# Optimization experiments

Measured on AMD Instinct MI355X. Metric: run time of the kernel, lower is better.

The kernel has to match this reference:

```python
import jax, jax.numpy as jnp
import numpy as np

LN_EPS = 1e-5

def _layernorm(x, g, b):
    mu = jnp.mean(x, axis=-1, keepdims=True)
    var = jnp.mean(jnp.square(x - mu), axis=-1, keepdims=True)
    return (x - mu) * jax.lax.rsqrt(var + LN_EPS) * g + b


def setup_inputs() -> dict:
    key = jax.random.key(0)
    ks = jax.random.split(key, 8)
    B, N, F = 2, 100000, 128
    E, G = 400000, 10
    EMB, C = 32, 128
    features = jax.random.normal(ks[0], (B, N, F), dtype=jnp.float32)
    edge_index = jax.random.randint(ks[1], (2, E), 0, N, dtype=jnp.int32)
    lengths = jnp.full((G,), N // G, dtype=jnp.int32)
    emb_table = jax.random.normal(ks[2], (128, EMB), dtype=jnp.float32)
    W_in = jax.random.normal(ks[3], (F - 1 + EMB, C), dtype=jnp.float32) * (1.0 / np.sqrt(F - 1 + EMB))
    b_in = jnp.zeros((C,), jnp.float32)
    g_in = jnp.ones((C,), jnp.float32)
    beta_in = jnp.zeros((C,), jnp.float32)
    msg_W = jax.random.normal(ks[4], (3, C, C), dtype=jnp.float32) * (1.0 / np.sqrt(C))
    msg_b = jnp.zeros((3, C), jnp.float32)
    msg_g = jnp.ones((3, C), jnp.float32)
    msg_beta = jnp.zeros((3, C), jnp.float32)
    W_proj = jax.random.normal(ks[5], (C, 1), dtype=jnp.float32) * (1.0 / np.sqrt(C))
    b_proj = jnp.zeros((1,), jnp.float32)
    return {"features": features, "edge_index": edge_index, "lengths": lengths,
            "emb_table": emb_table, "W_in": W_in, "b_in": b_in, "g_in": g_in, "beta_in": beta_in,
            "msg_W": msg_W, "msg_b": msg_b, "msg_g": msg_g, "msg_beta": msg_beta,
            "W_proj": W_proj, "b_proj": b_proj}


def reference(features, edge_index, lengths, emb_table, W_in, b_in, g_in, beta_in,
              msg_W, msg_b, msg_g, msg_beta, W_proj, b_proj):
    B, N, F = features.shape
    rows, cols = edge_index[0], edge_index[1]

    # row-normalized sparse adjacency values (no grad path in original: torch.no_grad)
    ones = jnp.ones(rows.shape[0], dtype=features.dtype)
    deg = jax.ops.segment_sum(ones, rows, num_segments=N)
    vals = 1.0 / jnp.clip(deg, 1.0)[rows]  # [E]
    vals = jax.lax.stop_gradient(vals)

    # embedding input layer
    op = jnp.clip(features[..., 0].astype(jnp.int32), 0, emb_table.shape[0] - 1)  # [B,N]
    x = jnp.concatenate([emb_table[op], features[..., 1:]], axis=-1)  # [B,N,F-1+emb]
    x = _layernorm(jax.nn.silu(x @ W_in + b_in), g_in, beta_in)  # [B,N,C]

    # sparse message passing: agg[i] = sum_j A[i,j] x[j]
    for l in range(msg_W.shape[0]):
        msg = x[:, cols, :] * vals[None, :, None]  # [B,E,C]
        agg = jnp.zeros_like(x).at[:, rows, :].add(msg)  # scatter-sum to rows
        x = _layernorm(jax.nn.silu(agg @ msg_W[l] + msg_b[l]), msg_g[l], msg_beta[l])

    # ragged graph pooling over node axis
    G = lengths.shape[0]
    index = jnp.asarray(np.repeat(np.arange(G), np.asarray(lengths)))  # [N]
    pooled = jax.ops.segment_sum(x.transpose(1, 0, 2), index, num_segments=G)  # [G,B,C]
    runtimes = pooled @ W_proj + b_proj  # [G,B,1]
    return runtimes[..., 0]  # [G,B]
```

## Files before the change

kernel.cpp:

```cpp
#include <hip/hip_runtime.h>
#include <cstddef>

#define LN_EPS 1e-5f
typedef unsigned short u16;
typedef unsigned int u32;
typedef __attribute__((ext_vector_type(8))) short bf16x8;
typedef __attribute__((ext_vector_type(4))) float f32x4;

constexpr int SCAN_T = 256, SCAN_V = 8, SCAN_ELEMS = SCAN_T * SCAN_V;
constexpr int KP = 136;

__device__ inline u16 f2bf(float f) {
    u32 u = __float_as_uint(f);
    u += 0x7FFFu + ((u >> 16) & 1u);
    return (u16)(u >> 16);
}
__device__ inline float bf2f(u16 h) { return __uint_as_float((u32)h << 16); }

__device__ inline void acc_u4(float* a, uint4 u) {
    a[0] += bf2f((u16)(u.x & 0xFFFF)); a[1] += bf2f((u16)(u.x >> 16));
    a[2] += bf2f((u16)(u.y & 0xFFFF)); a[3] += bf2f((u16)(u.y >> 16));
    a[4] += bf2f((u16)(u.z & 0xFFFF)); a[5] += bf2f((u16)(u.z >> 16));
    a[6] += bf2f((u16)(u.w & 0xFFFF)); a[7] += bf2f((u16)(u.w >> 16));
}

__global__ __launch_bounds__(256) void k_deg(const int* __restrict__ rows,
                                             int* __restrict__ deg, int E) {
    int e = blockIdx.x * 256 + threadIdx.x;
    if (e < E) atomicAdd(&deg[rows[e]], 1);
}

__global__ __launch_bounds__(256) void k_invdeg(const int* __restrict__ deg,
                                                float* __restrict__ invdeg, int N) {
    int i = blockIdx.x * 256 + threadIdx.x;
    if (i < N) invdeg[i] = 1.0f / (float)max(deg[i], 1);
}

__global__ __launch_bounds__(SCAN_T) void k_scan1(const int* __restrict__ deg,
                                                  int* __restrict__ row_ptr,
                                                  int* __restrict__ bsum, int N) {
    __shared__ int ts[SCAN_T];
    int t = threadIdx.x;
    int base = blockIdx.x * SCAN_ELEMS;
    int v[SCAN_V];
    int s = 0;
    #pragma unroll
    for (int j = 0; j < SCAN_V; ++j) {
        int i = base + t * SCAN_V + j;
        v[j] = (i < N) ? deg[i] : 0;
        s += v[j];
    }
    ts[t] = s;
    __syncthreads();
    for (int off = 1; off < SCAN_T; off <<= 1) {
        int val = (t >= off) ? ts[t - off] : 0;
        __syncthreads();
        ts[t] += val;
        __syncthreads();
    }
    int excl = (t > 0) ? ts[t - 1] : 0;
    #pragma unroll
    for (int j = 0; j < SCAN_V; ++j) {
        int i = base + t * SCAN_V + j;
        if (i < N) row_ptr[i] = excl;
        excl += v[j];
    }
    if (t == SCAN_T - 1) bsum[blockIdx.x] = ts[SCAN_T - 1];
}

__global__ void k_scan2(int* __restrict__ bsum, int nb, int* __restrict__ row_ptr, int N) {
    int run = 0;
    for (int i = 0; i < nb; ++i) {
        int v = bsum[i];
        bsum[i] = run;
        run += v;
    }
    row_ptr[N] = run;
}

__global__ __launch_bounds__(SCAN_T) void k_scan3(int* __restrict__ row_ptr,
                                                  const int* __restrict__ bsum, int N) {
    int add = bsum[blockIdx.x];
    int base = blockIdx.x * SCAN_ELEMS;
    #pragma unroll
    for (int j = 0; j < SCAN_V; ++j) {
        int i = base + threadIdx.x * SCAN_V + j;
        if (i < N) row_ptr[i] += add;
    }
}

__global__ __launch_bounds__(256) void k_copy_cursor(const int* __restrict__ row_ptr,
                                                     int* __restrict__ cursor, int N) {
    int i = blockIdx.x * 256 + threadIdx.x;
    if (i < N) cursor[i] = row_ptr[i];
}

__global__ __launch_bounds__(256) void k_bucket(const int* __restrict__ rows,
                                                const int* __restrict__ cols,
                                                int* __restrict__ cursor,
                                                int* __restrict__ col_sorted, int E) {
    int e = blockIdx.x * 256 + threadIdx.x;
    if (e < E) {
        int r = rows[e];
        int pos = atomicAdd(&cursor[r], 1);
        col_sorted[pos] = cols[e];
    }
}

__global__ __launch_bounds__(256) void k_wprep(const float* __restrict__ W_in,
                                               const float* __restrict__ msg_W,
                                               u16* __restrict__ Wt_in,
                                               u16* __restrict__ Wt_msg) {
    int idx = blockIdx.x * 256 + threadIdx.x;
    const int t1 = 128 * 128;
    if (idx < t1) {
        int c = idx >> 7, k = idx & 127;
        float v = (k >= 1) ? W_in[(31 + k) * 128 + c] : 0.f;
        Wt_in[idx] = f2bf(v);
    } else {
        idx -= t1;
        if (idx < 3 * 128 * 128) {
            int l = idx / (128 * 128);
            int r = idx & (128 * 128 - 1);
            int c = r >> 7, k = r & 127;
            Wt_msg[idx] = f2bf(msg_W[l * 16384 + k * 128 + c]);
        }
    }
}

__global__ __launch_bounds__(128) void k_eproj(const float* __restrict__ W_in,
                                               const float* __restrict__ emb,
                                               float* __restrict__ E_proj) {
    __shared__ float es[32];
    int op = blockIdx.x, c = threadIdx.x;
    if (c < 32) es[c] = emb[op * 32 + c];
    __syncthreads();
    float s = 0.f;
    #pragma unroll
    for (int j = 0; j < 32; ++j) s = fmaf(es[j], W_in[j * 128 + c], s);
    E_proj[op * 128 + c] = s;
}

__global__ __launch_bounds__(256) void k_input_mfma(
    const float* __restrict__ features, const float* __restrict__ E_proj,
    const u16* __restrict__ Wt,
    const float* __restrict__ bias, const float* __restrict__ gain,
    const float* __restrict__ beta, u16* __restrict__ x, int N, int ntiles)
{
    __shared__ u16 A[64 * KP];
    __shared__ u16 Wl[128 * KP];
    __shared__ int ops[64];
    const int tid = threadIdx.x;
    const int lane = tid & 63, w = tid >> 6;
    const int l15 = lane & 15;
    const int kq = (lane >> 4) * 8;
    const int r = tid >> 2, q = tid & 3;

    for (int i = tid; i < 2048; i += 256) {
        uint4 v = ((const uint4*)Wt)[i];
        *(uint4*)&Wl[(i >> 4) * KP + (i & 15) * 8] = v;
    }
    float bsr[8], gsr[8], btr[8];
    #pragma unroll
    for (int t = 0; t < 8; ++t) {
        int col = t * 16 + l15;
        bsr[t] = bias[col]; gsr[t] = gain[col]; btr[t] = beta[col];
    }

    for (int tile = blockIdx.x; tile < ntiles; tile += gridDim.x) {
        const int node0 = tile * 32;
        __syncthreads();
        {
            int nl = r >> 1, b = r & 1;
            int node = min(node0 + nl, N - 1);
            const float* fr = features + ((size_t)b * N + node) * 128 + q * 32;
            u32 pk[16];
            float4 v0 = ((const float4*)fr)[0];
            if (q == 0) {
                int op = (int)v0.x;
                op = op < 0 ? 0 : (op > 127 ? 127 : op);
                ops[r] = op;
            }
            pk[0] = (u32)f2bf(v0.x) | ((u32)f2bf(v0.y) << 16);
            pk[1] = (u32)f2bf(v0.z) | ((u32)f2bf(v0.w) << 16);
            #pragma unroll
            for (int j = 1; j < 8; ++j) {
                float4 v = ((const float4*)fr)[j];
                pk[2 * j]     = (u32)f2bf(v.x) | ((u32)f2bf(v.y) << 16);
                pk[2 * j + 1] = (u32)f2bf(v.z) | ((u32)f2bf(v.w) << 16);
            }
            uint4* dst = (uint4*)&A[r * KP + q * 32];
            #pragma unroll
            for (int j = 0; j < 4; ++j)
                dst[j] = make_uint4(pk[4 * j], pk[4 * j + 1], pk[4 * j + 2], pk[4 * j + 3]);
        }
        __syncthreads();

        const int arow = w * 16 + l15;
        bf16x8 a[4];
        #pragma unroll
        for (int kt = 0; kt < 4; ++kt)
            a[kt] = *(const bf16x8*)&A[arow * KP + kt * 32 + kq];
        f32x4 acc[8];
        #pragma unroll
        for (int t = 0; t < 8; ++t) {
            f32x4 c4 = {0.f, 0.f, 0.f, 0.f};
            #pragma unroll
            for (int kt = 0; kt < 4; ++kt) {
                bf16x8 b = *(const bf16x8*)&Wl[(t * 16 + l15) * KP + kt * 32 + kq];
                c4 = __builtin_amdgcn_mfma_f32_16x16x32_bf16(a[kt], b, c4, 0, 0, 0);
            }
            acc[t] = c4;
        }

        int opr[4];
        #pragma unroll
        for (int i = 0; i < 4; ++i) opr[i] = ops[w * 16 + (lane >> 4) * 4 + i];

        float s[4] = {0, 0, 0, 0}, sq[4] = {0, 0, 0, 0};
        #pragma unroll
        for (int t = 0; t < 8; ++t) {
            int col = t * 16 + l15;
            #pragma unroll
            for (int i = 0; i < 4; ++i) {
                float aY = acc[t][i] + bsr[t] + E_proj[opr[i] * 128 + col];
                float y = aY / (1.0f + __expf(-aY));
                acc[t][i] = y;
                s[i] += y;
                sq[i] = fmaf(y, y, sq[i]);
            }
        }
        #pragma unroll
        for (int m = 1; m <= 8; m <<= 1) {
            #pragma unroll
            for (int i = 0; i < 4; ++i) {
                s[i] += __shfl_xor(s[i], m);
                sq[i] += __shfl_xor(sq[i], m);
            }
        }
        #pragma unroll
        for (int i = 0; i < 4; ++i) {
            float mu = s[i] * (1.0f / 128.0f);
            float var = sq[i] * (1.0f / 128.0f) - mu * mu;
            float inv = rsqrtf(var + LN_EPS);
            int rr = w * 16 + (lane >> 4) * 4 + i;
            if (node0 + (rr >> 1) < N) {
                u16* xr = x + ((size_t)node0 * 2 + rr) * 128;
                #pragma unroll
                for (int t = 0; t < 8; ++t)
                    xr[t * 16 + l15] = f2bf((acc[t][i] - mu) * inv * gsr[t] + btr[t]);
            }
        }
    }
}

__global__ __launch_bounds__(512) void k_mp_mfma(
    const int* __restrict__ row_ptr, const int* __restrict__ col_sorted,
    const float* __restrict__ invdeg, const u16* __restrict__ xin,
    const u16* __restrict__ Wt, const float* __restrict__ bias,
    const float* __restrict__ gain, const float* __restrict__ beta,
    u16* __restrict__ xout, int N, int ntiles)
{
    __shared__ u16 A[64 * KP];
    __shared__ u16 Wl[128 * KP];
    __shared__ float pS[64][2], pQ[64][2];
    const int tid = threadIdx.x;
    const int lane = tid & 63, w = tid >> 6;
    const int l15 = lane & 15;
    const int kq = (lane >> 4) * 8;
    const int r = tid >> 3, sl = tid & 7;
    const int wr = w & 3, wc = w >> 2;

    for (int i = tid; i < 2048; i += 512) {
        uint4 v = ((const uint4*)Wt)[i];
        *(uint4*)&Wl[(i >> 4) * KP + (i & 15) * 8] = v;
    }

    for (int tile = blockIdx.x; tile < ntiles; tile += gridDim.x) {
        const int node0 = tile * 32;
        {
            int nl = r >> 1, b = r & 1;
            int node = min(node0 + nl, N - 1);
            int e0 = row_ptr[node], e1 = row_ptr[node + 1];
            float sc = invdeg[node];
            const u32* xb = (const u32*)xin + (size_t)b * 64 + sl * 8;
            float fa[16];
            #pragma unroll
            for (int j = 0; j < 16; ++j) fa[j] = 0.f;
            int e = e0;
            for (; e + 2 <= e1; e += 2) {
                int c0 = col_sorted[e], c1 = col_sorted[e + 1];
                const uint4* p0 = (const uint4*)(xb + (size_t)c0 * 128);
                const uint4* p1 = (const uint4*)(xb + (size_t)c1 * 128);
                uint4 u0 = p0[0], u1 = p0[1];
                uint4 w0 = p1[0], w1 = p1[1];
                acc_u4(fa, u0);     acc_u4(fa + 8, u1);
                acc_u4(fa, w0);     acc_u4(fa + 8, w1);
            }
            if (e < e1) {
                const uint4* p0 = (const uint4*)(xb + (size_t)col_sorted[e] * 128);
                uint4 u0 = p0[0], u1 = p0[1];
                acc_u4(fa, u0);     acc_u4(fa + 8, u1);
            }
            u32 pk[8];
            #pragma unroll
            for (int j = 0; j < 8; ++j)
                pk[j] = (u32)f2bf(fa[2 * j] * sc) | ((u32)f2bf(fa[2 * j + 1] * sc) << 16);
            uint4* dst = (uint4*)&A[r * KP + sl * 16];
            dst[0] = make_uint4(pk[0], pk[1], pk[2], pk[3]);
            dst[1] = make_uint4(pk[4], pk[5], pk[6], pk[7]);
        }
        __syncthreads();

        const int arow = wr * 16 + l15;
        bf16x8 a[4];
        #pragma unroll
        for (int kt = 0; kt < 4; ++kt)
            a[kt] = *(const bf16x8*)&A[arow * KP + kt * 32 + kq];
        f32x4 acc[4];
        #pragma unroll
        for (int t = 0; t < 4; ++t) {
            int bcol = wc * 64 + t * 16 + l15;
            f32x4 c4 = {0.f, 0.f, 0.f, 0.f};
            #pragma unroll
            for (int kt = 0; kt < 4; ++kt) {
                bf16x8 bfr = *(const bf16x8*)&Wl[bcol * KP + kt * 32 + kq];
                c4 = __builtin_amdgcn_mfma_f32_16x16x32_bf16(a[kt], bfr, c4, 0, 0, 0);
            }
            acc[t] = c4;
        }

        float s[4] = {0, 0, 0, 0}, sq[4] = {0, 0, 0, 0};
        #pragma unroll
        for (int t = 0; t < 4; ++t) {
            int col = wc * 64 + t * 16 + l15;
            float bt = bias[col];
            #pragma unroll
            for (int i = 0; i < 4; ++i) {
                float aY = acc[t][i] + bt;
                float y = aY / (1.0f + __expf(-aY));
                acc[t][i] = y;
                s[i] += y;
                sq[i] = fmaf(y, y, sq[i]);
            }
        }
        #pragma unroll
        for (int m = 1; m <= 8; m <<= 1) {
            #pragma unroll
            for (int i = 0; i < 4; ++i) {
                s[i] += __shfl_xor(s[i], m);
                sq[i] += __shfl_xor(sq[i], m);
            }
        }
        if (l15 == 0) {
            #pragma unroll
            for (int i = 0; i < 4; ++i) {
                int rr = wr * 16 + (lane >> 4) * 4 + i;
                pS[rr][wc] = s[i];
                pQ[rr][wc] = sq[i];
            }
        }
        __syncthreads();

        #pragma unroll
        for (int i = 0; i < 4; ++i) {
            int rr = wr * 16 + (lane >> 4) * 4 + i;
            float st = pS[rr][0] + pS[rr][1];
            float qt = pQ[rr][0] + pQ[rr][1];
            float mu = st * (1.0f / 128.0f);
            float var = qt * (1.0f / 128.0f) - mu * mu;
            float inv = rsqrtf(var + LN_EPS);
            if (node0 + (rr >> 1) < N) {
                u16* xr = xout + ((size_t)node0 * 2 + rr) * 128;
                #pragma unroll
                for (int t = 0; t < 4; ++t) {
                    int col = wc * 64 + t * 16 + l15;
                    xr[col] = f2bf((acc[t][i] - mu) * inv * gain[col] + beta[col]);
                }
            }
        }
    }
}

__global__ __launch_bounds__(64) void k_pool(
    const u16* __restrict__ x, const int* __restrict__ lengths,
    float* __restrict__ pooled, int N, int B, int G, int SPLIT)
{
    int blk = blockIdx.x;
    int split = blk % SPLIT;
    int gb = blk / SPLIT;
    int b = gb % B, g = gb / B;
    int lane = threadIdx.x;
    int start = 0;
    for (int i = 0; i < g; ++i) start += lengths[i];
    int len = lengths[g];
    int chunk = (len + SPLIT - 1) / SPLIT;
    int n0 = start + split * chunk;
    int n1 = min(start + len, n0 + chunk);
    const u32* xb = (const u32*)x + (size_t)b * 64;
    float sx = 0.f, sy = 0.f;
    int n = n0;
    for (; n + 4 <= n1; n += 4) {
        u32 v0 = xb[(size_t)(n + 0) * 128 + lane];
        u32 v1 = xb[(size_t)(n + 1) * 128 + lane];
        u32 v2 = xb[(size_t)(n + 2) * 128 + lane];
        u32 v3 = xb[(size_t)(n + 3) * 128 + lane];
        sx += bf2f((u16)(v0 & 0xFFFF)) + bf2f((u16)(v1 & 0xFFFF)) +
              bf2f((u16)(v2 & 0xFFFF)) + bf2f((u16)(v3 & 0xFFFF));
        sy += bf2f((u16)(v0 >> 16)) + bf2f((u16)(v1 >> 16)) +
              bf2f((u16)(v2 >> 16)) + bf2f((u16)(v3 >> 16));
    }
    for (; n < n1; ++n) {
        u32 v = xb[(size_t)n * 128 + lane];
        sx += bf2f((u16)(v & 0xFFFF));
        sy += bf2f((u16)(v >> 16));
    }
    if (n1 > n0) {
        atomicAdd(&pooled[(g * B + b) * 128 + lane * 2 + 0], sx);
        atomicAdd(&pooled[(g * B + b) * 128 + lane * 2 + 1], sy);
    }
}

__global__ __launch_bounds__(128) void k_proj(
    const float* __restrict__ pooled, const float* __restrict__ Wp,
    const float* __restrict__ bp, float* __restrict__ out, int GB)
{
    int gb = blockIdx.x;
    int tid = threadIdx.x;
    float v = pooled[gb * 128 + tid] * Wp[tid];
    v += __shfl_down(v, 32);
    v += __shfl_down(v, 16);
    v += __shfl_down(v, 8);
    v += __shfl_down(v, 4);
    v += __shfl_down(v, 2);
    v += __shfl_down(v, 1);
    __shared__ float red[2];
    if ((tid & 63) == 0) red[tid >> 6] = v;
    __syncthreads();
    if (tid == 0) out[gb] = red[0] + red[1] + bp[0];
}

extern "C" void kernel_launch(void* const* d_in, const int* in_sizes, int n_in,
                              void* d_out, int out_size, void* d_ws, size_t ws_size,
                              hipStream_t stream) {
    const float* features = (const float*)d_in[0];
    const int* edge_index = (const int*)d_in[1];
    const int* lengths    = (const int*)d_in[2];
    const float* emb      = (const float*)d_in[3];
    const float* W_in     = (const float*)d_in[4];
    const float* b_in     = (const float*)d_in[5];
    const float* g_in     = (const float*)d_in[6];
    const float* beta_in  = (const float*)d_in[7];
    const float* msg_W    = (const float*)d_in[8];
    const float* msg_b    = (const float*)d_in[9];
    const float* msg_g    = (const float*)d_in[10];
    const float* msg_beta = (const float*)d_in[11];
    const float* W_proj   = (const float*)d_in[12];
    const float* b_proj   = (const float*)d_in[13];
    float* out = (float*)d_out;

    const int E = in_sizes[1] / 2;
    const int G = in_sizes[2];
    const int B = out_size / G;
    const int C = in_sizes[5];
    const int F = 128;
    const int N = in_sizes[0] / (B * F);
    const int M = B * N;
    const int L = in_sizes[9] / C;

    const int* rows = edge_index;
    const int* cols = edge_index + E;

    u16* buf0   = (u16*)d_ws;
    u16* buf1   = buf0 + (size_t)M * 128;
    u16* Wt_in  = buf1 + (size_t)M * 128;
    u16* Wt_msg = Wt_in + 128 * 128;
    float* E_proj = (float*)(Wt_msg + 3 * 128 * 128);
    float* invdeg = E_proj + 128 * 128;
    int*   deg    = (int*)(invdeg + N);
    float* pooled = (float*)(deg + N);
    int*   row_ptr = (int*)(pooled + (size_t)G * B * 128);
    int*   col_sorted = row_ptr + N + 1;
    int*   bsum   = col_sorted + E;

    const int nb_scan = (N + SCAN_ELEMS - 1) / SCAN_ELEMS;
    const int nt32 = (N + 31) / 32;
    const int grid_mp = nt32 < 1024 ? nt32 : 1024;

    {
        int total = 4 * 128 * 128;
        k_wprep<<<(total + 255) / 256, 256, 0, stream>>>(W_in, msg_W, Wt_in, Wt_msg);
        k_eproj<<<128, 128, 0, stream>>>(W_in, emb, E_proj);
    }

    hipMemsetAsync(deg, 0, (size_t)N * sizeof(int), stream);
    k_deg<<<(E + 255) / 256, 256, 0, stream>>>(rows, deg, E);
    k_invdeg<<<(N + 255) / 256, 256, 0, stream>>>(deg, invdeg, N);
    k_scan1<<<nb_scan, SCAN_T, 0, stream>>>(deg, row_ptr, bsum, N);
    k_scan2<<<1, 1, 0, stream>>>(bsum, nb_scan, row_ptr, N);
    k_scan3<<<nb_scan, SCAN_T, 0, stream>>>(row_ptr, bsum, N);
    k_copy_cursor<<<(N + 255) / 256, 256, 0, stream>>>(row_ptr, deg, N);
    k_bucket<<<(E + 255) / 256, 256, 0, stream>>>(rows, cols, deg, col_sorted, E);

    k_input_mfma<<<grid_mp, 256, 0, stream>>>(features, E_proj, Wt_in,
                                              b_in, g_in, beta_in, buf0, N, nt32);

    u16* bufs[2] = {buf0, buf1};
    int cur = 0;
    for (int l = 0; l < L; ++l) {
        k_mp_mfma<<<grid_mp, 512, 0, stream>>>(row_ptr, col_sorted, invdeg,
                                               bufs[cur], Wt_msg + (size_t)l * 128 * 128,
                                               msg_b + (size_t)l * C, msg_g + (size_t)l * C,
                                               msg_beta + (size_t)l * C,
                                               bufs[1 - cur], N, nt32);
        cur = 1 - cur;
    }

    const int SPLIT = 128;
    hipMemsetAsync(pooled, 0, (size_t)G * B * 128 * sizeof(float), stream);
    k_pool<<<G * B * SPLIT, 64, 0, stream>>>(bufs[cur], lengths, pooled, N, B, G, SPLIT);
    k_proj<<<G * B, 128, 0, stream>>>(pooled, W_proj, b_proj, out, G * B);
}
```

Measured before the change: 338.0 us.

## Split input-layer columns across two wave groups with 512-thread blocks

The input MFMA kernel moves from 256 to 512 threads per block. Each wave now computes 64 of the 128 output columns for 16 rows, and the feature load is spread over 8 threads per row instead of 4. LayerNorm row statistics are combined across the two column halves through shared memory with an added barrier, and the barrier at the top of the tile loop is dropped. The aim is more parallelism and less register pressure per thread, at the cost of a shared-memory reduction and bias/gain/beta reads from global memory inside the loop instead of registers.

```diff
diff --git a/kernel.cpp b/kernel.cpp
--- a/kernel.cpp
+++ b/kernel.cpp
@@ -141,7 +141,7 @@
     E_proj[op * 128 + c] = s;
 }
 
-__global__ __launch_bounds__(256) void k_input_mfma(
+__global__ __launch_bounds__(512) void k_input_mfma(
     const float* __restrict__ features, const float* __restrict__ E_proj,
     const u16* __restrict__ Wt,
     const float* __restrict__ bias, const float* __restrict__ gain,
@@ -150,64 +150,62 @@
     __shared__ u16 A[64 * KP];
     __shared__ u16 Wl[128 * KP];
     __shared__ int ops[64];
+    __shared__ float pS[64][2], pQ[64][2];
     const int tid = threadIdx.x;
     const int lane = tid & 63, w = tid >> 6;
     const int l15 = lane & 15;
     const int kq = (lane >> 4) * 8;
-    const int r = tid >> 2, q = tid & 3;
-
-    for (int i = tid; i < 2048; i += 256) {
+    const int r = tid >> 3, sl = tid & 7;
+    const int wr = w & 3, wc = w >> 2;
+
+    for (int i = tid; i < 2048; i += 512) {
         uint4 v = ((const uint4*)Wt)[i];
         *(uint4*)&Wl[(i >> 4) * KP + (i & 15) * 8] = v;
     }
-    float bsr[8], gsr[8], btr[8];
-    #pragma unroll
-    for (int t = 0; t < 8; ++t) {
-        int col = t * 16 + l15;
-        bsr[t] = bias[col]; gsr[t] = gain[col]; btr[t] = beta[col];
-    }
 
     for (int tile = blockIdx.x; tile < ntiles; tile += gridDim.x) {
         const int node0 = tile * 32;
-        __syncthreads();
         {
             int nl = r >> 1, b = r & 1;
             int node = min(node0 + nl, N - 1);
-            const float* fr = features + ((size_t)b * N + node) * 128 + q * 32;
-            u32 pk[16];
+            const float* fr = features + ((size_t)b * N + node) * 128 + sl * 16;
             float4 v0 = ((const float4*)fr)[0];
-            if (q == 0) {
+            float4 v1 = ((const float4*)fr)[1];
+            float4 v2 = ((const float4*)fr)[2];
+            float4 v3 = ((const float4*)fr)[3];
+            if (sl == 0) {
                 int op = (int)v0.x;
                 op = op < 0 ? 0 : (op > 127 ? 127 : op);
                 ops[r] = op;
             }
+            u32 pk[8];
             pk[0] = (u32)f2bf(v0.x) | ((u32)f2bf(v0.y) << 16);
             pk[1] = (u32)f2bf(v0.z) | ((u32)f2bf(v0.w) << 16);
-            #pragma unroll
-            for (int j = 1; j < 8; ++j) {
-                float4 v = ((const float4*)fr)[j];
-                pk[2 * j]     = (u32)f2bf(v.x) | ((u32)f2bf(v.y) << 16);
-                pk[2 * j + 1] = (u32)f2bf(v.z) | ((u32)f2bf(v.w) << 16);
-            }
-            uint4* dst = (uint4*)&A[r * KP + q * 32];
-            #pragma unroll
-            for (int j = 0; j < 4; ++j)
-                dst[j] = make_uint4(pk[4 * j], pk[4 * j + 1], pk[4 * j + 2], pk[4 * j + 3]);
+            pk[2] = (u32)f2bf(v1.x) | ((u32)f2bf(v1.y) << 16);
+            pk[3] = (u32)f2bf(v1.z) | ((u32)f2bf(v1.w) << 16);
+            pk[4] = (u32)f2bf(v2.x) | ((u32)f2bf(v2.y) << 16);
+            pk[5] = (u32)f2bf(v2.z) | ((u32)f2bf(v2.w) << 16);
+            pk[6] = (u32)f2bf(v3.x) | ((u32)f2bf(v3.y) << 16);
+            pk[7] = (u32)f2bf(v3.z) | ((u32)f2bf(v3.w) << 16);
+            uint4* dst = (uint4*)&A[r * KP + sl * 16];
+            dst[0] = make_uint4(pk[0], pk[1], pk[2], pk[3]);
+            dst[1] = make_uint4(pk[4], pk[5], pk[6], pk[7]);
         }
         __syncthreads();
 
-        const int arow = w * 16 + l15;
+        const int arow = wr * 16 + l15;
         bf16x8 a[4];
         #pragma unroll
         for (int kt = 0; kt < 4; ++kt)
             a[kt] = *(const bf16x8*)&A[arow * KP + kt * 32 + kq];
-        f32x4 acc[8];
-        #pragma unroll
-        for (int t = 0; t < 8; ++t) {
+        f32x4 acc[4];
+        #pragma unroll
+        for (int t = 0; t < 4; ++t) {
+            int bcol = wc * 64 + t * 16 + l15;
             f32x4 c4 = {0.f, 0.f, 0.f, 0.f};
             #pragma unroll
             for (int kt = 0; kt < 4; ++kt) {
-                bf16x8 b = *(const bf16x8*)&Wl[(t * 16 + l15) * KP + kt * 32 + kq];
+                bf16x8 b = *(const bf16x8*)&Wl[bcol * KP + kt * 32 + kq];
                 c4 = __builtin_amdgcn_mfma_f32_16x16x32_bf16(a[kt], b, c4, 0, 0, 0);
             }
             acc[t] = c4;
@@ -215,15 +213,16 @@
 
         int opr[4];
         #pragma unroll
-        for (int i = 0; i < 4; ++i) opr[i] = ops[w * 16 + (lane >> 4) * 4 + i];
+        for (int i = 0; i < 4; ++i) opr[i] = ops[wr * 16 + (lane >> 4) * 4 + i];
 
         float s[4] = {0, 0, 0, 0}, sq[4] = {0, 0, 0, 0};
         #pragma unroll
-        for (int t = 0; t < 8; ++t) {
-            int col = t * 16 + l15;
+        for (int t = 0; t < 4; ++t) {
+            int col = wc * 64 + t * 16 + l15;
+            float bt = bias[col];
             #pragma unroll
             for (int i = 0; i < 4; ++i) {
-                float aY = acc[t][i] + bsr[t] + E_proj[opr[i] * 128 + col];
+                float aY = acc[t][i] + bt + E_proj[opr[i] * 128 + col];
                 float y = aY / (1.0f + __expf(-aY));
                 acc[t][i] = y;
                 s[i] += y;
@@ -238,17 +237,31 @@
                 sq[i] += __shfl_xor(sq[i], m);
             }
         }
+        if (l15 == 0) {
+            #pragma unroll
+            for (int i = 0; i < 4; ++i) {
+                int rr = wr * 16 + (lane >> 4) * 4 + i;
+                pS[rr][wc] = s[i];
+                pQ[rr][wc] = sq[i];
+            }
+        }
+        __syncthreads();
+
         #pragma unroll
         for (int i = 0; i < 4; ++i) {
-            float mu = s[i] * (1.0f / 128.0f);
-            float var = sq[i] * (1.0f / 128.0f) - mu * mu;
+            int rr = wr * 16 + (lane >> 4) * 4 + i;
+            float st = pS[rr][0] + pS[rr][1];
+            float qt = pQ[rr][0] + pQ[rr][1];
+            float mu = st * (1.0f / 128.0f);
+            float var = qt * (1.0f / 128.0f) - mu * mu;
             float inv = rsqrtf(var + LN_EPS);
-            int rr = w * 16 + (lane >> 4) * 4 + i;
             if (node0 + (rr >> 1) < N) {
                 u16* xr = x + ((size_t)node0 * 2 + rr) * 128;
                 #pragma unroll
-                for (int t = 0; t < 8; ++t)
-                    xr[t * 16 + l15] = f2bf((acc[t][i] - mu) * inv * gsr[t] + btr[t]);
+                for (int t = 0; t < 4; ++t) {
+                    int col = wc * 64 + t * 16 + l15;
+                    xr[col] = f2bf((acc[t][i] - mu) * inv * gain[col] + beta[col]);
+                }
             }
         }
     }
@@ -502,7 +515,7 @@
     k_copy_cursor<<<(N + 255) / 256, 256, 0, stream>>>(row_ptr, deg, N);
     k_bucket<<<(E + 255) / 256, 256, 0, stream>>>(rows, cols, deg, col_sorted, E);
 
-    k_input_mfma<<<grid_mp, 256, 0, stream>>>(features, E_proj, Wt_in,
+    k_input_mfma<<<grid_mp, 512, 0, stream>>>(features, E_proj, Wt_in,
                                               b_in, g_in, beta_in, buf0, N, nt32);
 
     u16* bufs[2] = {buf0, buf1};
```

New measurement: 335.5 us. About the same (-0.8%).
